# Kernel tuning notes

Measured on AMD Instinct MI355X. Metric: run time of the kernel, lower is better.

## Reference

```python
import jax, jax.numpy as jnp
import numpy as np

B, T, D, H, TE = 4, 2048, 1024, 8, 2048
EPS = 1e-5

def _ln(x, w, b):
    m = jnp.mean(x, axis=-1, keepdims=True)
    v = jnp.mean((x - m) ** 2, axis=-1, keepdims=True)
    return (x - m) * jax.lax.rsqrt(v + EPS) * w + b

def setup_inputs() -> dict:
    key = jax.random.key(0)
    ks = jax.random.split(key, 16)
    s = 0.02
    inp = {
        'x': jax.random.normal(ks[0], (B, T, D), jnp.float32),
        'emb': jax.random.normal(ks[1], (B, TE), jnp.float32),
        'src_mask': (jax.random.uniform(ks[2], (B, T, 1)) > 0.2).astype(jnp.float32),
        'num_head': H,
        'ln_w': jnp.ones((D,), jnp.float32),
        'ln_b': jnp.zeros((D,), jnp.float32),
        'Wq': jax.random.normal(ks[3], (D, D), jnp.float32) * s,
        'bq': jnp.zeros((D,), jnp.float32),
        'Wk': jax.random.normal(ks[4], (D, D), jnp.float32) * s,
        'bk': jnp.zeros((D,), jnp.float32),
        'Wv': jax.random.normal(ks[5], (D, D), jnp.float32) * s,
        'bv': jnp.zeros((D,), jnp.float32),
        'W_emb': jax.random.normal(ks[6], (TE, 2 * D), jnp.float32) * s,
        'b_emb': jnp.zeros((2 * D,), jnp.float32),
        'ln2_w': jnp.ones((D,), jnp.float32),
        'ln2_b': jnp.zeros((D,), jnp.float32),
        'W_out': jax.random.normal(ks[7], (D, D), jnp.float32) * s,
        'b_out': jnp.zeros((D,), jnp.float32),
    }
    return inp

def reference(x, emb, src_mask, num_head, ln_w, ln_b, Wq, bq, Wk, bk, Wv, bv,
              W_emb, b_emb, ln2_w, ln2_b, W_out, b_out):
    b, t, d = x.shape
    h = num_head
    dh = d // h
    xn = _ln(x, ln_w, ln_b)
    q = xn @ Wq + bq
    k = xn @ Wk + bk + (1.0 - src_mask) * -1000000.0
    q = jax.nn.softmax(q.reshape(b, t, h, dh), axis=-1)   # feature-map softmax over d_head
    k = jax.nn.softmax(k.reshape(b, t, h, dh), axis=1)    # softmax over time
    v = ((xn @ Wv + bv) * src_mask).reshape(b, t, h, dh)
    att = jnp.einsum('bnhd,bnhl->bhdl', k, v)             # [B,H,dh,dh] KV summary
    y = jnp.einsum('bnhd,bhdl->bnhl', q, att).reshape(b, t, d)
    # StylizationBlock (FiLM), dropout p=0
    emb_out = (jax.nn.silu(emb) @ W_emb + b_emb)[:, None, :]  # [B,1,2D]
    scale, shift = jnp.split(emb_out, 2, axis=2)
    hh = _ln(y, ln2_w, ln2_b) * (1.0 + scale) + shift
    hh = jax.nn.silu(hh) @ W_out + b_out
    return x + hh
```

## Files before the change

kernel.cpp:

```cpp
#include <hip/hip_runtime.h>
#include <hip/hip_bf16.h>

#define B_  4
#define T_  2048
#define D_  1024
#define H_  8
#define DH_ 128
#define TE_ 2048
#define M_  (B_*T_)

using short8 = __attribute__((ext_vector_type(8))) short;
using f32x4  = __attribute__((ext_vector_type(4))) float;

__device__ __forceinline__ ushort f2bf(float f) {
  union { float f; unsigned u; } v; v.f = f;
  unsigned r = (v.u + 0x7fffu + ((v.u >> 16) & 1u)) >> 16;
  return (ushort)r;
}
__device__ __forceinline__ float bf2f(ushort h) {
  union { unsigned u; float f; } v; v.u = ((unsigned)h) << 16;
  return v.f;
}

#define GLOAD_LDS16(g, l) __builtin_amdgcn_global_load_lds( \
    (const __attribute__((address_space(1))) void*)(g), \
    (__attribute__((address_space(3))) void*)(l), 16, 0, 0)

__device__ __forceinline__ void gemm_mainloop(
    const ushort* __restrict__ A, int lda,
    const ushort* __restrict__ Bt, int ldb,
    int K, ushort (*As)[128*32], ushort (*Bs)[128*32], f32x4 acc[4][4])
{
  const int tid  = threadIdx.x;
  const int lane = tid & 63;
  const int wave = tid >> 6;
  const int row  = tid >> 2;
  const int ck   = (tid & 3) * 8;
  const int wm   = (wave & 1) * 64;
  const int wn   = (wave >> 1) * 64;
  const int fr   = lane & 15;
  const int quad = lane >> 4;

  const ushort* ga0 = A  + (size_t)row*lda + ck;
  const ushort* ga1 = A  + (size_t)(row+64)*lda + ck;
  const ushort* gb0 = Bt + (size_t)row*ldb + ck;
  const ushort* gb1 = Bt + (size_t)(row+64)*ldb + ck;
  const int woff = wave*512;

  for (int k0 = 0; k0 < K; k0 += 64) {
    GLOAD_LDS16(ga0 + k0,      As[0] + woff);
    GLOAD_LDS16(ga1 + k0,      As[0] + 2048 + woff);
    GLOAD_LDS16(gb0 + k0,      Bs[0] + woff);
    GLOAD_LDS16(gb1 + k0,      Bs[0] + 2048 + woff);
    GLOAD_LDS16(ga0 + k0 + 32, As[1] + woff);
    GLOAD_LDS16(ga1 + k0 + 32, As[1] + 2048 + woff);
    GLOAD_LDS16(gb0 + k0 + 32, Bs[1] + woff);
    GLOAD_LDS16(gb1 + k0 + 32, Bs[1] + 2048 + woff);
    __syncthreads();
    short8 af[2][4], bw[2][4];
#pragma unroll
    for (int c = 0; c < 2; ++c)
#pragma unroll
      for (int i = 0; i < 4; ++i) {
        af[c][i] = *(const short8*)&As[c][(wm + i*16 + fr)*32 + quad*8];
        bw[c][i] = *(const short8*)&Bs[c][(wn + i*16 + fr)*32 + quad*8];
      }
#pragma unroll
    for (int c = 0; c < 2; ++c)
#pragma unroll
      for (int i = 0; i < 4; ++i)
#pragma unroll
        for (int j = 0; j < 4; ++j)
          acc[i][j] = __builtin_amdgcn_mfma_f32_16x16x32_bf16(af[c][i], bw[c][j], acc[i][j], 0, 0, 0);
    __syncthreads();
  }
}

__global__ __launch_bounds__(256) void gemm_qkv_kernel(
    const ushort* __restrict__ xn, const ushort* __restrict__ Wt,
    const float* __restrict__ bq, const float* __restrict__ bk,
    const float* __restrict__ bv, const float* __restrict__ mask,
    ushort* __restrict__ q, ushort* __restrict__ kT, ushort* __restrict__ vT,
    float* __restrict__ ksum)
{
  __shared__ __align__(16) ushort As[2][128*32], Bs[2][128*32];
  const int m0 = blockIdx.x * 128;
  const int nt = blockIdx.y;
  f32x4 acc[4][4] = {};
  gemm_mainloop(xn + (size_t)m0*D_, D_, Wt + (size_t)nt*128*D_, D_, D_, As, Bs, acc);

  const int tid = threadIdx.x;
  const int lane = tid & 63, wave = tid >> 6;
  const int wm = (wave & 1)*64, wn = (wave >> 1)*64;
  const int fr = lane & 15, quad = lane >> 4;
  const int grp = nt >> 3;
  const int h = nt & 7;
  const int hbase = h*DH_;

  if (grp == 0) {
    float* redm = (float*)As;
    float* reds = (float*)As + 256;
    const int wi = wn >> 6;
    float bb[4];
#pragma unroll
    for (int j = 0; j < 4; ++j) bb[j] = bq[hbase + wn + j*16 + fr];
#pragma unroll
    for (int i = 0; i < 4; ++i)
#pragma unroll
      for (int r = 0; r < 4; ++r) {
        float m = -1e30f;
#pragma unroll
        for (int j = 0; j < 4; ++j) m = fmaxf(m, acc[i][j][r] + bb[j]);
        m = fmaxf(m, __shfl_xor(m, 1, 64));
        m = fmaxf(m, __shfl_xor(m, 2, 64));
        m = fmaxf(m, __shfl_xor(m, 4, 64));
        m = fmaxf(m, __shfl_xor(m, 8, 64));
        if (fr == 0) redm[(wm + i*16 + quad*4 + r)*2 + wi] = m;
      }
    __syncthreads();
#pragma unroll
    for (int i = 0; i < 4; ++i)
#pragma unroll
      for (int r = 0; r < 4; ++r) {
        int R = wm + i*16 + quad*4 + r;
        float gm = fmaxf(redm[R*2], redm[R*2+1]);
        float s = 0.f;
#pragma unroll
        for (int j = 0; j < 4; ++j) {
          float e = __expf(acc[i][j][r] + bb[j] - gm);
          acc[i][j][r] = e; s += e;
        }
        s += __shfl_xor(s, 1, 64);
        s += __shfl_xor(s, 2, 64);
        s += __shfl_xor(s, 4, 64);
        s += __shfl_xor(s, 8, 64);
        if (fr == 0) reds[R*2 + wi] = s;
      }
    __syncthreads();
#pragma unroll
    for (int i = 0; i < 4; ++i)
#pragma unroll
      for (int r = 0; r < 4; ++r) {
        int R = wm + i*16 + quad*4 + r;
        float inv = 1.0f / (reds[R*2] + reds[R*2+1]);
        size_t m = (size_t)(m0 + R);
#pragma unroll
        for (int j = 0; j < 4; ++j)
          q[m*D_ + hbase + wn + j*16 + fr] = f2bf(acc[i][j][r] * inv);
      }
  } else {
    const float* bias = (grp == 1) ? bk : bv;
    ushort* dstT = (grp == 1) ? kT : vT;
    const int b = m0 >> 11;
    const int t_in_b = m0 & (T_-1);
#pragma unroll
    for (int j = 0; j < 4; ++j) {
      int col = wn + j*16 + fr;
      float bb = bias[hbase + col];
      float sj = 0.f;
#pragma unroll
      for (int i = 0; i < 4; ++i) {
        int t0 = t_in_b + wm + i*16 + quad*4;
        ushort4 pk; ushort* pp = (ushort*)&pk;
#pragma unroll
        for (int r = 0; r < 4; ++r) {
          int m = m0 + wm + i*16 + quad*4 + r;
          float v = acc[i][j][r] + bb;
          if (grp == 1) {
            v = __expf(v + (1.0f - mask[m]) * -1000000.0f);
            sj += v;
          } else {
            v *= mask[m];
          }
          pp[r] = f2bf(v);
        }
        *(ushort4*)&dstT[((size_t)(b*H_ + h)*DH_ + col)*T_ + t0] = pk;
      }
      if (grp == 1) {
        sj += __shfl_xor(sj, 16, 64);
        sj += __shfl_xor(sj, 32, 64);
        if (quad == 0) atomicAdd(&ksum[(b*H_ + h)*DH_ + col], sj);
      }
    }
  }
}

__global__ __launch_bounds__(256) void gemm_att_kernel(
    const ushort* __restrict__ kT, const ushort* __restrict__ vT,
    const float* __restrict__ ksum, ushort* __restrict__ attT)
{
  __shared__ __align__(16) ushort As[2][128*32], Bs[2][128*32];
  const int bh = blockIdx.x;
  f32x4 acc[4][4] = {};
  gemm_mainloop(kT + (size_t)bh*DH_*T_, T_,
                vT + (size_t)bh*DH_*T_, T_, T_, As, Bs, acc);
  const int tid = threadIdx.x, lane = tid & 63, wave = tid >> 6;
  const int wm = (wave & 1)*64, wn = (wave >> 1)*64, fr = lane & 15, quad = lane >> 4;
  const float* ks = ksum + bh*DH_;
#pragma unroll
  for (int i = 0; i < 4; ++i)
#pragma unroll
    for (int j = 0; j < 4; ++j) {
      int l = wn + j*16 + fr;
      int d0 = wm + i*16 + quad*4;
      ushort4 pk; ushort* pp = (ushort*)&pk;
#pragma unroll
      for (int r = 0; r < 4; ++r) pp[r] = f2bf(acc[i][j][r] / ks[d0 + r]);
      *(ushort4*)&attT[((size_t)bh*DH_ + l)*DH_ + d0] = pk;
    }
}

__global__ __launch_bounds__(256) void gemm_y_kernel(
    const ushort* __restrict__ q, const ushort* __restrict__ attT,
    ushort* __restrict__ y)
{
  __shared__ __align__(16) ushort As[2][128*32], Bs[2][128*32];
  const int mt = blockIdx.x;
  const int bh = blockIdx.y;
  const int b = bh >> 3, h = bh & 7;
  const int m0 = b*T_ + mt*128;
  f32x4 acc[4][4] = {};
  gemm_mainloop(q + (size_t)m0*D_ + h*DH_, D_,
                attT + (size_t)bh*DH_*DH_, DH_, DH_, As, Bs, acc);
  const int tid = threadIdx.x, lane = tid & 63, wave = tid >> 6;
  const int wm = (wave & 1)*64, wn = (wave >> 1)*64, fr = lane & 15, quad = lane >> 4;
#pragma unroll
  for (int i = 0; i < 4; ++i)
#pragma unroll
    for (int j = 0; j < 4; ++j) {
      int l = wn + j*16 + fr;
#pragma unroll
      for (int r = 0; r < 4; ++r) {
        int m = m0 + wm + i*16 + quad*4 + r;
        y[(size_t)m*D_ + h*DH_ + l] = f2bf(acc[i][j][r]);
      }
    }
}

__global__ __launch_bounds__(256) void gemm_out_kernel(
    const ushort* __restrict__ act, const ushort* __restrict__ WoutT,
    const float* __restrict__ b_out, const float* __restrict__ x,
    float* __restrict__ out)
{
  __shared__ __align__(16) ushort As[2][128*32], Bs[2][128*32];
  const int m0 = blockIdx.x*128, n0 = blockIdx.y*128;
  f32x4 acc[4][4] = {};
  gemm_mainloop(act + (size_t)m0*D_, D_, WoutT + (size_t)n0*D_, D_, D_, As, Bs, acc);
  const int tid = threadIdx.x, lane = tid & 63, wave = tid >> 6;
  const int wm = (wave & 1)*64, wn = (wave >> 1)*64, fr = lane & 15, quad = lane >> 4;
#pragma unroll
  for (int i = 0; i < 4; ++i)
#pragma unroll
    for (int j = 0; j < 4; ++j) {
      int col = n0 + wn + j*16 + fr;
      float bb = b_out[col];
#pragma unroll
      for (int r = 0; r < 4; ++r) {
        int m = m0 + wm + i*16 + quad*4 + r;
        out[(size_t)m*D_ + col] = acc[i][j][r] + bb + x[(size_t)m*D_ + col];
      }
    }
}

__global__ __launch_bounds__(256) void ln1_kernel(
    const float* __restrict__ x, const float* __restrict__ w,
    const float* __restrict__ bb, ushort* __restrict__ xn)
{
  __shared__ float red[8];
  const int row = blockIdx.x, tid = threadIdx.x;
  const int lane = tid & 63, wave = tid >> 6;
  float4 v = *(const float4*)&x[(size_t)row*D_ + tid*4];
  float s  = v.x + v.y + v.z + v.w;
  float sq = v.x*v.x + v.y*v.y + v.z*v.z + v.w*v.w;
#pragma unroll
  for (int off = 32; off; off >>= 1) { s += __shfl_xor(s, off, 64); sq += __shfl_xor(sq, off, 64); }
  if (lane == 0) { red[wave] = s; red[4+wave] = sq; }
  __syncthreads();
  s  = red[0] + red[1] + red[2] + red[3];
  sq = red[4] + red[5] + red[6] + red[7];
  float mean = s * (1.0f/D_);
  float var  = sq * (1.0f/D_) - mean*mean;
  float rstd = rsqrtf(var + 1e-5f);
  int c = tid*4;
  float vv[4] = {v.x, v.y, v.z, v.w};
  ushort4 o; ushort* op = (ushort*)&o;
#pragma unroll
  for (int i = 0; i < 4; ++i) op[i] = f2bf((vv[i]-mean)*rstd*w[c+i] + bb[c+i]);
  *(ushort4*)&xn[(size_t)row*D_ + c] = o;
}

__global__ __launch_bounds__(256) void ln2_film_kernel(
    const ushort* __restrict__ y, const float* __restrict__ w,
    const float* __restrict__ bb, const float* __restrict__ film,
    const float* __restrict__ b_emb, ushort* __restrict__ act)
{
  __shared__ float red[8];
  const int row = blockIdx.x, tid = threadIdx.x;
  const int lane = tid & 63, wave = tid >> 6;
  const int b = row >> 11;
  ushort4 raw = *(const ushort4*)&y[(size_t)row*D_ + tid*4];
  ushort* u = (ushort*)&raw;
  float v[4];
  float s = 0.f, sq = 0.f;
#pragma unroll
  for (int i = 0; i < 4; ++i) { v[i] = bf2f(u[i]); s += v[i]; sq += v[i]*v[i]; }
#pragma unroll
  for (int off = 32; off; off >>= 1) { s += __shfl_xor(s, off, 64); sq += __shfl_xor(sq, off, 64); }
  if (lane == 0) { red[wave] = s; red[4+wave] = sq; }
  __syncthreads();
  s  = red[0] + red[1] + red[2] + red[3];
  sq = red[4] + red[5] + red[6] + red[7];
  float mean = s * (1.0f/D_);
  float var  = sq * (1.0f/D_) - mean*mean;
  float rstd = rsqrtf(var + 1e-5f);
  int c = tid*4;
  ushort4 o; ushort* op = (ushort*)&o;
#pragma unroll
  for (int i = 0; i < 4; ++i) {
    float yn = (v[i]-mean)*rstd*w[c+i] + bb[c+i];
    float scale = film[b*2048 + c+i]        + b_emb[c+i];
    float shift = film[b*2048 + 1024 + c+i] + b_emb[1024 + c+i];
    float hh = yn*(1.f + scale) + shift;
    op[i] = f2bf(hh / (1.f + __expf(-hh)));
  }
  *(ushort4*)&act[(size_t)row*D_ + c] = o;
}

__global__ __launch_bounds__(256) void film_kernel(
    const float* __restrict__ emb, const float* __restrict__ W_emb,
    float* __restrict__ film)
{
  __shared__ float se[4][64];
  const int tid = threadIdx.x;
  const int j  = blockIdx.x*256 + tid;
  const int t0 = blockIdx.y*64;
  { int b = tid >> 6, tt = tid & 63;
    float e = emb[b*TE_ + t0 + tt];
    se[b][tt] = e / (1.f + __expf(-e)); }
  __syncthreads();
  float a0 = 0.f, a1 = 0.f, a2 = 0.f, a3 = 0.f;
#pragma unroll 8
  for (int tt = 0; tt < 64; ++tt) {
    float wv = W_emb[(size_t)(t0 + tt)*2048 + j];
    a0 += se[0][tt]*wv; a1 += se[1][tt]*wv;
    a2 += se[2][tt]*wv; a3 += se[3][tt]*wv;
  }
  atomicAdd(&film[0*2048 + j], a0);
  atomicAdd(&film[1*2048 + j], a1);
  atomicAdd(&film[2*2048 + j], a2);
  atomicAdd(&film[3*2048 + j], a3);
}

__global__ __launch_bounds__(256) void prep_w_kernel(
    const float* __restrict__ Wq, const float* __restrict__ Wk,
    const float* __restrict__ Wv, const float* __restrict__ Wout,
    ushort* __restrict__ Wqkvt, ushort* __restrict__ WoutT)
{
  __shared__ float tile[32][33];
  const int z = blockIdx.z;
  const float* S = (z == 0) ? Wq : (z == 1) ? Wk : (z == 2) ? Wv : Wout;
  ushort* Dst = (z < 3) ? (Wqkvt + (size_t)z*D_*D_) : WoutT;
  const int n0 = blockIdx.x*32, k0 = blockIdx.y*32;
  const int tx = threadIdx.x & 31, ty = threadIdx.x >> 5;
#pragma unroll
  for (int i = 0; i < 4; ++i)
    tile[ty + i*8][tx] = S[(size_t)(k0 + ty + i*8)*D_ + n0 + tx];
  __syncthreads();
#pragma unroll
  for (int i = 0; i < 4; ++i)
    Dst[(size_t)(n0 + ty + i*8)*D_ + k0 + tx] = f2bf(tile[tx][ty + i*8]);
}

extern "C" void kernel_launch(void* const* d_in, const int* in_sizes, int n_in,
                              void* d_out, int out_size, void* d_ws, size_t ws_size,
                              hipStream_t stream)
{
  const float* x     = (const float*)d_in[0];
  const float* emb   = (const float*)d_in[1];
  const float* mask  = (const float*)d_in[2];
  const float* ln_w  = (const float*)d_in[4];
  const float* ln_b  = (const float*)d_in[5];
  const float* Wq    = (const float*)d_in[6];
  const float* bq    = (const float*)d_in[7];
  const float* Wk    = (const float*)d_in[8];
  const float* bk    = (const float*)d_in[9];
  const float* Wv    = (const float*)d_in[10];
  const float* bv    = (const float*)d_in[11];
  const float* W_emb = (const float*)d_in[12];
  const float* b_emb = (const float*)d_in[13];
  const float* ln2_w = (const float*)d_in[14];
  const float* ln2_b = (const float*)d_in[15];
  const float* Wout  = (const float*)d_in[16];
  const float* b_out = (const float*)d_in[17];
  float* out = (float*)d_out;

  char* ws = (char*)d_ws;
  size_t off = 0;
  auto alloc = [&](size_t bytes) { void* p = ws + off; off += (bytes + 255) & ~size_t(255); return p; };
  ushort* xn    = (ushort*)alloc((size_t)M_*D_*2);
  ushort* q     = (ushort*)alloc((size_t)M_*D_*2);
  ushort* kT    = (ushort*)alloc((size_t)M_*D_*2);
  ushort* vT    = (ushort*)alloc((size_t)M_*D_*2);
  ushort* y     = (ushort*)alloc((size_t)M_*D_*2);
  ushort* Wqkvt = (ushort*)alloc((size_t)3*D_*D_*2);
  ushort* WoutT = (ushort*)alloc((size_t)D_*D_*2);
  ushort* attT  = (ushort*)alloc((size_t)B_*H_*DH_*DH_*2);
  float*  film  = (float*)alloc((size_t)B_*2*D_*4);
  float*  ksum  = (float*)alloc((size_t)B_*H_*DH_*4);
  ushort* act   = xn;

  hipMemsetAsync(film, 0, (size_t)(B_*2*D_ + B_*H_*DH_)*4, stream);
  prep_w_kernel<<<dim3(32, 32, 4), 256, 0, stream>>>(Wq, Wk, Wv, Wout, Wqkvt, WoutT);
  film_kernel<<<dim3(8, 32), 256, 0, stream>>>(emb, W_emb, film);
  ln1_kernel<<<M_, 256, 0, stream>>>(x, ln_w, ln_b, xn);
  gemm_qkv_kernel<<<dim3(64, 24), 256, 0, stream>>>(xn, Wqkvt, bq, bk, bv, mask, q, kT, vT, ksum);
  gemm_att_kernel<<<32, 256, 0, stream>>>(kT, vT, ksum, attT);
  gemm_y_kernel<<<dim3(16, 32), 256, 0, stream>>>(q, attT, y);
  ln2_film_kernel<<<M_, 256, 0, stream>>>(y, ln2_w, ln2_b, film, b_emb, act);
  gemm_out_kernel<<<dim3(64, 8), 256, 0, stream>>>(act, WoutT, b_out, x, out);
}
```

Before: 309.0 us.

## Split-K the KV summary GEMM and merge prologue kernels into one launch

The KV summary GEMM previously ran only 32 blocks, each walking the full time dimension. It now splits time into 8 chunks, writes fp32 partial results into scratch reused from the y buffer, and a new reduction kernel sums the partials, divides by ksum and converts to bf16. Separately, LayerNorm1, the weight transpose/convert and the FiLM matvec are merged into a single launch that dispatches on block index. The goal is better GPU occupancy on the small GEMM and less launch overhead, at the cost of an extra kernel and extra fp32 traffic for the partials.

```diff
diff --git a/kernel.cpp b/kernel.cpp
--- a/kernel.cpp
+++ b/kernel.cpp
@@ -187,27 +187,46 @@
 
 __global__ __launch_bounds__(256) void gemm_att_kernel(
     const ushort* __restrict__ kT, const ushort* __restrict__ vT,
-    const float* __restrict__ ksum, ushort* __restrict__ attT)
+    float* __restrict__ P)
 {
   __shared__ __align__(16) ushort As[2][128*32], Bs[2][128*32];
   const int bh = blockIdx.x;
+  const int s  = blockIdx.y;
   f32x4 acc[4][4] = {};
-  gemm_mainloop(kT + (size_t)bh*DH_*T_, T_,
-                vT + (size_t)bh*DH_*T_, T_, T_, As, Bs, acc);
+  gemm_mainloop(kT + (size_t)bh*DH_*T_ + s*256, T_,
+                vT + (size_t)bh*DH_*T_ + s*256, T_, 256, As, Bs, acc);
   const int tid = threadIdx.x, lane = tid & 63, wave = tid >> 6;
   const int wm = (wave & 1)*64, wn = (wave >> 1)*64, fr = lane & 15, quad = lane >> 4;
-  const float* ks = ksum + bh*DH_;
+  float* Pb = P + ((size_t)(s*32 + bh))*DH_*DH_;
 #pragma unroll
   for (int i = 0; i < 4; ++i)
 #pragma unroll
     for (int j = 0; j < 4; ++j) {
       int l = wn + j*16 + fr;
       int d0 = wm + i*16 + quad*4;
-      ushort4 pk; ushort* pp = (ushort*)&pk;
-#pragma unroll
-      for (int r = 0; r < 4; ++r) pp[r] = f2bf(acc[i][j][r] / ks[d0 + r]);
-      *(ushort4*)&attT[((size_t)bh*DH_ + l)*DH_ + d0] = pk;
+      float4 pk = {acc[i][j][0], acc[i][j][1], acc[i][j][2], acc[i][j][3]};
+      *(float4*)&Pb[(size_t)l*DH_ + d0] = pk;
     }
+}
+
+__global__ __launch_bounds__(256) void att_reduce_kernel(
+    const float* __restrict__ P, const float* __restrict__ ksum,
+    ushort* __restrict__ attT)
+{
+  const int e = (blockIdx.x*256 + threadIdx.x) * 4;
+  float4 s = {0.f, 0.f, 0.f, 0.f};
+#pragma unroll
+  for (int k = 0; k < 8; ++k) {
+    float4 p = *(const float4*)&P[(size_t)k*32*DH_*DH_ + e];
+    s.x += p.x; s.y += p.y; s.z += p.z; s.w += p.w;
+  }
+  const int bh = e >> 14;
+  const int d  = e & 127;
+  const float4 ks = *(const float4*)&ksum[bh*DH_ + d];
+  ushort4 o; ushort* op = (ushort*)&o;
+  op[0] = f2bf(s.x / ks.x); op[1] = f2bf(s.y / ks.y);
+  op[2] = f2bf(s.z / ks.z); op[3] = f2bf(s.w / ks.w);
+  *(ushort4*)&attT[e] = o;
 }
 
 __global__ __launch_bounds__(256) void gemm_y_kernel(
@@ -262,33 +281,6 @@
     }
 }
 
-__global__ __launch_bounds__(256) void ln1_kernel(
-    const float* __restrict__ x, const float* __restrict__ w,
-    const float* __restrict__ bb, ushort* __restrict__ xn)
-{
-  __shared__ float red[8];
-  const int row = blockIdx.x, tid = threadIdx.x;
-  const int lane = tid & 63, wave = tid >> 6;
-  float4 v = *(const float4*)&x[(size_t)row*D_ + tid*4];
-  float s  = v.x + v.y + v.z + v.w;
-  float sq = v.x*v.x + v.y*v.y + v.z*v.z + v.w*v.w;
-#pragma unroll
-  for (int off = 32; off; off >>= 1) { s += __shfl_xor(s, off, 64); sq += __shfl_xor(sq, off, 64); }
-  if (lane == 0) { red[wave] = s; red[4+wave] = sq; }
-  __syncthreads();
-  s  = red[0] + red[1] + red[2] + red[3];
-  sq = red[4] + red[5] + red[6] + red[7];
-  float mean = s * (1.0f/D_);
-  float var  = sq * (1.0f/D_) - mean*mean;
-  float rstd = rsqrtf(var + 1e-5f);
-  int c = tid*4;
-  float vv[4] = {v.x, v.y, v.z, v.w};
-  ushort4 o; ushort* op = (ushort*)&o;
-#pragma unroll
-  for (int i = 0; i < 4; ++i) op[i] = f2bf((vv[i]-mean)*rstd*w[c+i] + bb[c+i]);
-  *(ushort4*)&xn[(size_t)row*D_ + c] = o;
-}
-
 __global__ __launch_bounds__(256) void ln2_film_kernel(
     const ushort* __restrict__ y, const float* __restrict__ w,
     const float* __restrict__ bb, const float* __restrict__ film,
@@ -326,49 +318,78 @@
   *(ushort4*)&act[(size_t)row*D_ + c] = o;
 }
 
-__global__ __launch_bounds__(256) void film_kernel(
+__global__ __launch_bounds__(256) void prologue_kernel(
+    const float* __restrict__ x, const float* __restrict__ lw,
+    const float* __restrict__ lb, ushort* __restrict__ xn,
+    const float* __restrict__ Wq, const float* __restrict__ Wk,
+    const float* __restrict__ Wv, const float* __restrict__ Wout,
+    ushort* __restrict__ Wqkvt, ushort* __restrict__ WoutT,
     const float* __restrict__ emb, const float* __restrict__ W_emb,
     float* __restrict__ film)
 {
-  __shared__ float se[4][64];
+  __shared__ float smem[32*33];
+  const int bid = blockIdx.x;
   const int tid = threadIdx.x;
-  const int j  = blockIdx.x*256 + tid;
-  const int t0 = blockIdx.y*64;
-  { int b = tid >> 6, tt = tid & 63;
-    float e = emb[b*TE_ + t0 + tt];
-    se[b][tt] = e / (1.f + __expf(-e)); }
-  __syncthreads();
-  float a0 = 0.f, a1 = 0.f, a2 = 0.f, a3 = 0.f;
+
+  if (bid < M_) {
+    const int row = bid;
+    const int lane = tid & 63, wave = tid >> 6;
+    float* red = smem;
+    float4 v = *(const float4*)&x[(size_t)row*D_ + tid*4];
+    float s  = v.x + v.y + v.z + v.w;
+    float sq = v.x*v.x + v.y*v.y + v.z*v.z + v.w*v.w;
+#pragma unroll
+    for (int off = 32; off; off >>= 1) { s += __shfl_xor(s, off, 64); sq += __shfl_xor(sq, off, 64); }
+    if (lane == 0) { red[wave] = s; red[4+wave] = sq; }
+    __syncthreads();
+    s  = red[0] + red[1] + red[2] + red[3];
+    sq = red[4] + red[5] + red[6] + red[7];
+    float mean = s * (1.0f/D_);
+    float var  = sq * (1.0f/D_) - mean*mean;
+    float rstd = rsqrtf(var + 1e-5f);
+    int c = tid*4;
+    float vv[4] = {v.x, v.y, v.z, v.w};
+    ushort4 o; ushort* op = (ushort*)&o;
+#pragma unroll
+    for (int i = 0; i < 4; ++i) op[i] = f2bf((vv[i]-mean)*rstd*lw[c+i] + lb[c+i]);
+    *(ushort4*)&xn[(size_t)row*D_ + c] = o;
+  } else if (bid < M_ + 4096) {
+    const int idx = bid - M_;
+    const int z = idx >> 10;
+    const int rem = idx & 1023;
+    const int n0 = (rem & 31)*32, k0 = (rem >> 5)*32;
+    const float* S = (z == 0) ? Wq : (z == 1) ? Wk : (z == 2) ? Wv : Wout;
+    ushort* Dst = (z < 3) ? (Wqkvt + (size_t)z*D_*D_) : WoutT;
+    float (*tile)[33] = (float(*)[33])smem;
+    const int tx = tid & 31, ty = tid >> 5;
+#pragma unroll
+    for (int i = 0; i < 4; ++i)
+      tile[ty + i*8][tx] = S[(size_t)(k0 + ty + i*8)*D_ + n0 + tx];
+    __syncthreads();
+#pragma unroll
+    for (int i = 0; i < 4; ++i)
+      Dst[(size_t)(n0 + ty + i*8)*D_ + k0 + tx] = f2bf(tile[tx][ty + i*8]);
+  } else {
+    const int idx = bid - M_ - 4096;
+    const int j  = (idx & 7)*256 + tid;
+    const int t0 = (idx >> 3)*64;
+    float (*se)[64] = (float(*)[64])smem;
+    { int b = tid >> 6, tt = tid & 63;
+      float e = emb[b*TE_ + t0 + tt];
+      se[b][tt] = e / (1.f + __expf(-e)); }
+    __syncthreads();
+    float a0 = 0.f, a1 = 0.f, a2 = 0.f, a3 = 0.f;
 #pragma unroll 8
-  for (int tt = 0; tt < 64; ++tt) {
-    float wv = W_emb[(size_t)(t0 + tt)*2048 + j];
-    a0 += se[0][tt]*wv; a1 += se[1][tt]*wv;
-    a2 += se[2][tt]*wv; a3 += se[3][tt]*wv;
+    for (int tt = 0; tt < 64; ++tt) {
+      float wv = W_emb[(size_t)(t0 + tt)*2048 + j];
+      a0 += se[0][tt]*wv; a1 += se[1][tt]*wv;
+      a2 += se[2][tt]*wv; a3 += se[3][tt]*wv;
+    }
+    atomicAdd(&film[0*2048 + j], a0);
+    atomicAdd(&film[1*2048 + j], a1);
+    atomicAdd(&film[2*2048 + j], a2);
+    atomicAdd(&film[3*2048 + j], a3);
   }
-  atomicAdd(&film[0*2048 + j], a0);
-  atomicAdd(&film[1*2048 + j], a1);
-  atomicAdd(&film[2*2048 + j], a2);
-  atomicAdd(&film[3*2048 + j], a3);
-}
-
-__global__ __launch_bounds__(256) void prep_w_kernel(
-    const float* __restrict__ Wq, const float* __restrict__ Wk,
-    const float* __restrict__ Wv, const float* __restrict__ Wout,
-    ushort* __restrict__ Wqkvt, ushort* __restrict__ WoutT)
-{
-  __shared__ float tile[32][33];
-  const int z = blockIdx.z;
-  const float* S = (z == 0) ? Wq : (z == 1) ? Wk : (z == 2) ? Wv : Wout;
-  ushort* Dst = (z < 3) ? (Wqkvt + (size_t)z*D_*D_) : WoutT;
-  const int n0 = blockIdx.x*32, k0 = blockIdx.y*32;
-  const int tx = threadIdx.x & 31, ty = threadIdx.x >> 5;
-#pragma unroll
-  for (int i = 0; i < 4; ++i)
-    tile[ty + i*8][tx] = S[(size_t)(k0 + ty + i*8)*D_ + n0 + tx];
-  __syncthreads();
-#pragma unroll
-  for (int i = 0; i < 4; ++i)
-    Dst[(size_t)(n0 + ty + i*8)*D_ + k0 + tx] = f2bf(tile[tx][ty + i*8]);
 }
 
 extern "C" void kernel_launch(void* const* d_in, const int* in_sizes, int n_in,
@@ -408,13 +429,14 @@
   float*  film  = (float*)alloc((size_t)B_*2*D_*4);
   float*  ksum  = (float*)alloc((size_t)B_*H_*DH_*4);
   ushort* act   = xn;
+  float*  P     = (float*)y;
 
   hipMemsetAsync(film, 0, (size_t)(B_*2*D_ + B_*H_*DH_)*4, stream);
-  prep_w_kernel<<<dim3(32, 32, 4), 256, 0, stream>>>(Wq, Wk, Wv, Wout, Wqkvt, WoutT);
-  film_kernel<<<dim3(8, 32), 256, 0, stream>>>(emb, W_emb, film);
-  ln1_kernel<<<M_, 256, 0, stream>>>(x, ln_w, ln_b, xn);
+  prologue_kernel<<<M_ + 4096 + 256, 256, 0, stream>>>(
+      x, ln_w, ln_b, xn, Wq, Wk, Wv, Wout, Wqkvt, WoutT, emb, W_emb, film);
   gemm_qkv_kernel<<<dim3(64, 24), 256, 0, stream>>>(xn, Wqkvt, bq, bk, bv, mask, q, kT, vT, ksum);
-  gemm_att_kernel<<<32, 256, 0, stream>>>(kT, vT, ksum, attT);
+  gemm_att_kernel<<<dim3(32, 8), 256, 0, stream>>>(kT, vT, P);
+  att_reduce_kernel<<<512, 256, 0, stream>>>(P, ksum, attT);
   gemm_y_kernel<<<dim3(16, 32), 256, 0, stream>>>(q, attT, y);
   ln2_film_kernel<<<M_, 256, 0, stream>>>(y, ln2_w, ln2_b, film, b_emb, act);
   gemm_out_kernel<<<dim3(64, 8), 256, 0, stream>>>(act, WoutT, b_out, x, out);
```

After: 280.7 us. -9.2%, faster.

## Split-K the KV-summary GEMM across time chunks with a separate reduction kernel

Applied to the files above, without the earlier changes.

The per-head K^T·V GEMM previously ran as only 32 blocks, each covering the full 2048-long time reduction, which leaves most of the GPU idle. It now splits the time dimension into 8 chunks of 256, giving 256 blocks. Each block writes fp32 partial results into a scratch buffer that aliases y. A new reduce kernel sums the partials, divides by ksum and writes bf16 attT. The cost is one extra launch and about 4 MB of fp32 partial traffic; the film launch order is also swapped.

```diff
diff --git a/kernel.cpp b/kernel.cpp
--- a/kernel.cpp
+++ b/kernel.cpp
@@ -187,27 +187,46 @@
 
 __global__ __launch_bounds__(256) void gemm_att_kernel(
     const ushort* __restrict__ kT, const ushort* __restrict__ vT,
-    const float* __restrict__ ksum, ushort* __restrict__ attT)
+    float* __restrict__ P)
 {
   __shared__ __align__(16) ushort As[2][128*32], Bs[2][128*32];
   const int bh = blockIdx.x;
+  const int s  = blockIdx.y;
   f32x4 acc[4][4] = {};
-  gemm_mainloop(kT + (size_t)bh*DH_*T_, T_,
-                vT + (size_t)bh*DH_*T_, T_, T_, As, Bs, acc);
+  gemm_mainloop(kT + (size_t)bh*DH_*T_ + s*256, T_,
+                vT + (size_t)bh*DH_*T_ + s*256, T_, 256, As, Bs, acc);
   const int tid = threadIdx.x, lane = tid & 63, wave = tid >> 6;
   const int wm = (wave & 1)*64, wn = (wave >> 1)*64, fr = lane & 15, quad = lane >> 4;
-  const float* ks = ksum + bh*DH_;
+  float* Pb = P + ((size_t)(s*32 + bh))*DH_*DH_;
 #pragma unroll
   for (int i = 0; i < 4; ++i)
 #pragma unroll
     for (int j = 0; j < 4; ++j) {
       int l = wn + j*16 + fr;
       int d0 = wm + i*16 + quad*4;
-      ushort4 pk; ushort* pp = (ushort*)&pk;
-#pragma unroll
-      for (int r = 0; r < 4; ++r) pp[r] = f2bf(acc[i][j][r] / ks[d0 + r]);
-      *(ushort4*)&attT[((size_t)bh*DH_ + l)*DH_ + d0] = pk;
+      float4 pk = {acc[i][j][0], acc[i][j][1], acc[i][j][2], acc[i][j][3]};
+      *(float4*)&Pb[(size_t)l*DH_ + d0] = pk;
     }
+}
+
+__global__ __launch_bounds__(256) void att_reduce_kernel(
+    const float* __restrict__ P, const float* __restrict__ ksum,
+    ushort* __restrict__ attT)
+{
+  const int e = (blockIdx.x*256 + threadIdx.x) * 4;
+  float4 s = {0.f, 0.f, 0.f, 0.f};
+#pragma unroll
+  for (int k = 0; k < 8; ++k) {
+    float4 p = *(const float4*)&P[(size_t)k*32*DH_*DH_ + e];
+    s.x += p.x; s.y += p.y; s.z += p.z; s.w += p.w;
+  }
+  const int bh = e >> 14;
+  const int d  = e & 127;
+  const float4 ks = *(const float4*)&ksum[bh*DH_ + d];
+  ushort4 o; ushort* op = (ushort*)&o;
+  op[0] = f2bf(s.x / ks.x); op[1] = f2bf(s.y / ks.y);
+  op[2] = f2bf(s.z / ks.z); op[3] = f2bf(s.w / ks.w);
+  *(ushort4*)&attT[e] = o;
 }
 
 __global__ __launch_bounds__(256) void gemm_y_kernel(
@@ -408,13 +427,15 @@
   float*  film  = (float*)alloc((size_t)B_*2*D_*4);
   float*  ksum  = (float*)alloc((size_t)B_*H_*DH_*4);
   ushort* act   = xn;
+  float*  P     = (float*)y;
 
   hipMemsetAsync(film, 0, (size_t)(B_*2*D_ + B_*H_*DH_)*4, stream);
+  film_kernel<<<dim3(8, 32), 256, 0, stream>>>(emb, W_emb, film);
   prep_w_kernel<<<dim3(32, 32, 4), 256, 0, stream>>>(Wq, Wk, Wv, Wout, Wqkvt, WoutT);
-  film_kernel<<<dim3(8, 32), 256, 0, stream>>>(emb, W_emb, film);
   ln1_kernel<<<M_, 256, 0, stream>>>(x, ln_w, ln_b, xn);
   gemm_qkv_kernel<<<dim3(64, 24), 256, 0, stream>>>(xn, Wqkvt, bq, bk, bv, mask, q, kT, vT, ksum);
-  gemm_att_kernel<<<32, 256, 0, stream>>>(kT, vT, ksum, attT);
+  gemm_att_kernel<<<dim3(32, 8), 256, 0, stream>>>(kT, vT, P);
+  att_reduce_kernel<<<512, 256, 0, stream>>>(P, ksum, attT);
   gemm_y_kernel<<<dim3(16, 32), 256, 0, stream>>>(q, attT, y);
   ln2_film_kernel<<<M_, 256, 0, stream>>>(y, ln2_w, ln2_b, film, b_emb, act);
   gemm_out_kernel<<<dim3(64, 8), 256, 0, stream>>>(act, WoutT, b_out, x, out);
```

New measurement: 282.5 us. -8.6%, faster.
